# Performance work log

Hardware: AMD Instinct MI355X
Metric: run time of the kernel (lower is better)

The kernel has to match this reference:

```python
import jax, jax.numpy as jnp
import numpy as np

B, S, D, H, DK, DV, F, L, V = 2, 1024, 1024, 16, 64, 64, 4096, 4, 32000
PAD = 0
EPS = 1e-5


def posenc(seq_len, dim):
    # sinusoidal positional encoding (dim even)
    pos = jnp.arange(seq_len, dtype=jnp.float32)[:, None]
    div = jnp.exp(-(jnp.arange(0, dim, 2, dtype=jnp.float32) / dim) * np.log(10000.0))
    pe = jnp.zeros((seq_len, dim), jnp.float32)
    pe = pe.at[:, 0::2].set(jnp.sin(pos * div))
    pe = pe.at[:, 1::2].set(jnp.cos(pos * div))
    return pe


def layer_norm(x, g, b):
    mu = jnp.mean(x, axis=-1, keepdims=True)
    var = jnp.mean((x - mu) ** 2, axis=-1, keepdims=True)
    return (x - mu) / jnp.sqrt(var + EPS) * g + b


def setup_inputs() -> dict:
    key = jax.random.key(0)
    ks = jax.random.split(key, 10)
    n = lambda k, shape: jax.random.normal(k, shape, jnp.float32) * 0.02
    return {
        "tokens": jax.random.randint(ks[0], (B, S), 0, V),
        "emb": n(ks[1], (V, D)),
        "Wq": n(ks[2], (L, D, H * DK)), "bq": jnp.zeros((L, H * DK), jnp.float32),
        "Wk": n(ks[3], (L, D, H * DK)), "bk": jnp.zeros((L, H * DK), jnp.float32),
        "Wv": n(ks[4], (L, D, H * DV)), "bv": jnp.zeros((L, H * DV), jnp.float32),
        "Wo": n(ks[5], (L, H * DV, D)), "bo": jnp.zeros((L, D), jnp.float32),
        "ln1_g": jnp.ones((L, D), jnp.float32), "ln1_b": jnp.zeros((L, D), jnp.float32),
        "W1": n(ks[6], (L, D, F)),
        "W2": n(ks[7], (L, F, D)),
        "ln2_g": jnp.ones((L, D), jnp.float32), "ln2_b": jnp.zeros((L, D), jnp.float32),
    }


def reference(tokens, emb, Wq, bq, Wk, bk, Wv, bv, Wo, bo,
              ln1_g, ln1_b, W1, W2, ln2_g, ln2_b):
    x = emb[tokens] + posenc(S, D)                      # [B,S,D]
    # pad mask from key sequence: True where key token == PAD, broadcast over heads/queries
    mask = (tokens == PAD)[:, None, None, :]            # [B,1,1,S]
    scale = 1.0 / np.sqrt(DK)
    for l in range(L):
        residual = x
        q = (x @ Wq[l] + bq[l]).reshape(B, S, H, DK).transpose(0, 2, 1, 3)  # [B,H,S,DK]
        k = (x @ Wk[l] + bk[l]).reshape(B, S, H, DK).transpose(0, 2, 1, 3)
        v = (x @ Wv[l] + bv[l]).reshape(B, S, H, DV).transpose(0, 2, 1, 3)
        scores = jnp.einsum('bhqd,bhkd->bhqk', q, k) * scale                # [B,H,S,S]
        scores = jnp.where(mask, -1e9, scores)
        attn = jax.nn.softmax(scores, axis=-1)
        ctx = jnp.einsum('bhqk,bhkd->bhqd', attn, v)                        # [B,H,S,DV]
        ctx = ctx.transpose(0, 2, 1, 3).reshape(B, S, H * DV)
        x = layer_norm(residual + ctx @ Wo[l] + bo[l], ln1_g[l], ln1_b[l])
        # position-wise FFN (linear mode, no bias, exact GELU)
        h = jax.nn.gelu(x @ W1[l], approximate=False)
        x = layer_norm(x + h @ W2[l], ln2_g[l], ln2_b[l])
    return x
```

## Files before the change

### kernel.cpp

```cpp
#include <hip/hip_runtime.h>
#include <math.h>

#define S_  1024
#define D_  1024
#define Hh  16
#define DKk 64
#define Bb  2
#define Ff  4096
#define Ll  4

typedef __bf16 bf16_t;
using bf16x4 = __attribute__((ext_vector_type(4))) __bf16;
using bf16x8 = __attribute__((ext_vector_type(8))) __bf16;
using f32x4  = __attribute__((ext_vector_type(4))) float;

#define AS1 __attribute__((address_space(1)))
#define AS3 __attribute__((address_space(3)))

__device__ __forceinline__ void gld_lds16(const bf16_t* g, bf16_t* l)
{
    __builtin_amdgcn_global_load_lds((AS1 void*)g, (AS3 void*)l, 16, 0, 0);
}

__global__ __launch_bounds__(256) void embed_kernel(const int* __restrict__ tokens,
                                                    const float* __restrict__ emb,
                                                    float* __restrict__ X,
                                                    bf16_t* __restrict__ Xh)
{
    const int row = blockIdx.x;
    const int s   = row & (S_ - 1);
    const int tok = tokens[row];
    const float* e = emb + (size_t)tok * D_;
    const float LN10000 = 9.210340371976184f;
    #pragma unroll
    for (int i = 0; i < 4; ++i) {
        int d = threadIdx.x + 256 * i;
        int half = d >> 1;
        float div = expf(-((float)(2 * half) / (float)D_) * LN10000);
        float ang = (float)s * div;
        float pe = (d & 1) ? cosf(ang) : sinf(ang);
        float v = e[d] + pe;
        X [(size_t)row * D_ + d] = v;
        Xh[(size_t)row * D_ + d] = (bf16_t)v;
    }
}

__global__ __launch_bounds__(256) void transpose_cast_kernel(const float* __restrict__ in,
                                                             bf16_t* __restrict__ out,
                                                             int K, int N)
{
    __shared__ float T[32][33];
    const int n0 = blockIdx.x * 32;
    const int k0 = blockIdx.y * 32;
    const int t  = threadIdx.x;
    const int r  = t >> 3;
    const int c  = (t & 7) * 4;

    float4 v = *(const float4*)(in + (size_t)(k0 + r) * N + n0 + c);
    T[r][c + 0] = v.x; T[r][c + 1] = v.y; T[r][c + 2] = v.z; T[r][c + 3] = v.w;
    __syncthreads();

    bf16x4 o = { (bf16_t)T[c + 0][r], (bf16_t)T[c + 1][r],
                 (bf16_t)T[c + 2][r], (bf16_t)T[c + 3][r] };
    *(bf16x4*)(out + (size_t)(n0 + r) * K + k0 + c) = o;
}

__global__ __launch_bounds__(256) void concat_bias_kernel(const float* __restrict__ bq,
                                                          const float* __restrict__ bk,
                                                          const float* __restrict__ bv,
                                                          float* __restrict__ out)
{
    const int id = blockIdx.x * 256 + threadIdx.x;
    const int l  = id / 3072;
    const int j  = id % 3072;
    float v;
    if (j < 1024)      v = bq[l * 1024 + j];
    else if (j < 2048) v = bk[l * 1024 + j - 1024];
    else               v = bv[l * 1024 + j - 2048];
    out[id] = v;
}

template<int BN>
__global__ __launch_bounds__(256) void gemm_bf16_kernel(const bf16_t* __restrict__ A,
                                                        const bf16_t* __restrict__ Bt,
                                                        const float* __restrict__ bias,
                                                        void* __restrict__ Cv,
                                                        int N, int K, int flags)
{
    constexpr int NI = BN / 32;
    __shared__ bf16_t As[128 * 32];
    __shared__ bf16_t Bs[BN * 32];

    const int t    = threadIdx.x;
    const int w    = t >> 6;
    const int lane = t & 63;
    const int l15  = lane & 15;
    const int q8   = lane >> 4;
    const int wm   = w >> 1;
    const int wn   = w & 1;

    const int bm = blockIdx.y * 128;
    const int bn = blockIdx.x * BN;

    const int lr4 = lane >> 2;
    const int lc8 = (lane & 3) * 8;

    f32x4 acc[4][NI] = {};

    for (int k0 = 0; k0 < K; k0 += 32) {
        #pragma unroll
        for (int u = 0; u < 2; ++u) {
            const int row0 = w * 32 + u * 16;
            gld_lds16(A + (size_t)(bm + row0 + lr4) * K + k0 + lc8,
                      As + row0 * 32);
        }
        #pragma unroll
        for (int u = 0; u < BN / 64; ++u) {
            const int row0 = w * (BN / 4) + u * 16;
            gld_lds16(Bt + (size_t)(bn + row0 + lr4) * K + k0 + lc8,
                      Bs + row0 * 32);
        }
        __syncthreads();

        bf16x8 af[4], bf[NI];
        #pragma unroll
        for (int mi = 0; mi < 4; ++mi)
            af[mi] = *(const bf16x8*)(As + (wm * 64 + mi * 16 + l15) * 32 + q8 * 8);
        #pragma unroll
        for (int ni = 0; ni < NI; ++ni)
            bf[ni] = *(const bf16x8*)(Bs + (wn * (NI * 16) + ni * 16 + l15) * 32 + q8 * 8);

        #pragma unroll
        for (int mi = 0; mi < 4; ++mi)
            #pragma unroll
            for (int ni = 0; ni < NI; ++ni)
                acc[mi][ni] = __builtin_amdgcn_mfma_f32_16x16x32_bf16(
                                  af[mi], bf[ni], acc[mi][ni], 0, 0, 0);
        __syncthreads();
    }

    #pragma unroll
    for (int mi = 0; mi < 4; ++mi) {
        #pragma unroll
        for (int ni = 0; ni < NI; ++ni) {
            const int n = bn + wn * (NI * 16) + ni * 16 + l15;
            const float bv_ = (flags & 1) ? bias[n] : 0.f;
            #pragma unroll
            for (int r = 0; r < 4; ++r) {
                const int m = bm + wm * 64 + mi * 16 + q8 * 4 + r;
                float v = acc[mi][ni][r] + bv_;
                if (flags & 2) v = 0.5f * v * (1.0f + erff(v * 0.70710678118654752f));
                if (flags & 4) ((bf16_t*)Cv)[(size_t)m * N + n] = (bf16_t)v;
                else           ((float*) Cv)[(size_t)m * N + n] = v;
            }
        }
    }
}

#define AST 72
#define LDQ 3072

__global__ __launch_bounds__(256) void attn_mfma_kernel(const bf16_t* __restrict__ QKV,
                                                        const int* __restrict__ tokens,
                                                        bf16_t* __restrict__ Octx)
{
    const int qt = blockIdx.x;
    const int h  = blockIdx.y;
    const int b  = blockIdx.z;
    const int t    = threadIdx.x;
    const int wave = t >> 6;
    const int lane = t & 63;
    const int l15  = lane & 15;
    const int q8   = lane >> 4;

    __shared__ bf16_t Ks[64][AST];
    __shared__ bf16_t VsT[64][AST];
    __shared__ bf16_t Ps[4][16][AST];

    const bf16_t* Qp = QKV + 0;
    const bf16_t* Kp = QKV + 1024;
    const bf16_t* Vp = QKV + 2048;

    const int q0 = qt * 64 + wave * 16;
    bf16x8 qf0, qf1;
    {
        const bf16_t* qp = Qp + ((size_t)(b * S_ + q0 + l15)) * LDQ + h * 64 + q8 * 8;
        qf0 = *(const bf16x8*)(qp);
        qf1 = *(const bf16x8*)(qp + 32);
    }

    f32x4 Oacc[4] = {};
    float m_run[4], l_run[4];
    #pragma unroll
    for (int r = 0; r < 4; ++r) { m_run[r] = -INFINITY; l_run[r] = 0.f; }

    for (int jt = 0; jt < S_ / 64; ++jt) {
        __syncthreads();
        {
            const bf16_t* kb = Kp + ((size_t)(b * S_ + jt * 64)) * LDQ + h * 64;
            #pragma unroll
            for (int u = 0; u < 2; ++u) {
                int id = t + 256 * u;
                int r  = id >> 3;
                int c  = (id & 7) * 8;
                *(uint4*)&Ks[r][c] = *(const uint4*)(kb + (size_t)r * LDQ + c);
            }
        }
        {
            const bf16_t* vb = Vp + ((size_t)(b * S_ + jt * 64)) * LDQ + h * 64;
            const int j  = lane;
            const int d0 = wave * 16;
            #pragma unroll
            for (int u = 0; u < 2; ++u) {
                bf16x8 vv = *(const bf16x8*)(vb + (size_t)j * LDQ + d0 + u * 8);
                #pragma unroll
                for (int e = 0; e < 8; ++e)
                    VsT[d0 + u * 8 + e][j] = vv[e];
            }
        }
        __syncthreads();

        float sc[4][4];
        #pragma unroll
        for (int nt = 0; nt < 4; ++nt) {
            const bf16_t* kp = &Ks[nt * 16 + l15][q8 * 8];
            bf16x8 b0 = *(const bf16x8*)(kp);
            bf16x8 b1 = *(const bf16x8*)(kp + 32);
            f32x4 a = {};
            a = __builtin_amdgcn_mfma_f32_16x16x32_bf16(qf0, b0, a, 0, 0, 0);
            a = __builtin_amdgcn_mfma_f32_16x16x32_bf16(qf1, b1, a, 0, 0, 0);
            const int jg = jt * 64 + nt * 16 + l15;
            const float msk = (tokens[b * S_ + jg] == 0) ? -1e9f : 0.f;
            #pragma unroll
            for (int r = 0; r < 4; ++r) sc[nt][r] = a[r] * 0.125f + msk;
        }

        float alpha[4];
        #pragma unroll
        for (int r = 0; r < 4; ++r) {
            float mx = fmaxf(fmaxf(sc[0][r], sc[1][r]), fmaxf(sc[2][r], sc[3][r]));
            #pragma unroll
            for (int o = 1; o < 16; o <<= 1) mx = fmaxf(mx, __shfl_xor(mx, o));
            const float mn = fmaxf(m_run[r], mx);
            alpha[r] = __expf(m_run[r] - mn);
            m_run[r] = mn;
            float s = 0.f;
            #pragma unroll
            for (int nt = 0; nt < 4; ++nt) {
                float p = __expf(sc[nt][r] - mn);
                sc[nt][r] = p;
                s += p;
            }
            #pragma unroll
            for (int o = 1; o < 16; o <<= 1) s += __shfl_xor(s, o);
            l_run[r] = l_run[r] * alpha[r] + s;
        }

        #pragma unroll
        for (int nt = 0; nt < 4; ++nt)
            #pragma unroll
            for (int r = 0; r < 4; ++r)
                Ps[wave][q8 * 4 + r][nt * 16 + l15] = (bf16_t)sc[nt][r];

        bf16x8 pf0 = *(const bf16x8*)&Ps[wave][l15][q8 * 8];
        bf16x8 pf1 = *(const bf16x8*)&Ps[wave][l15][32 + q8 * 8];

        #pragma unroll
        for (int dt = 0; dt < 4; ++dt) {
            #pragma unroll
            for (int r = 0; r < 4; ++r) Oacc[dt][r] *= alpha[r];
            const bf16_t* vp = &VsT[dt * 16 + l15][q8 * 8];
            bf16x8 v0 = *(const bf16x8*)(vp);
            bf16x8 v1 = *(const bf16x8*)(vp + 32);
            Oacc[dt] = __builtin_amdgcn_mfma_f32_16x16x32_bf16(pf0, v0, Oacc[dt], 0, 0, 0);
            Oacc[dt] = __builtin_amdgcn_mfma_f32_16x16x32_bf16(pf1, v1, Oacc[dt], 0, 0, 0);
        }
    }

    #pragma unroll
    for (int dt = 0; dt < 4; ++dt) {
        #pragma unroll
        for (int r = 0; r < 4; ++r) {
            const int qg = q0 + q8 * 4 + r;
            Octx[((size_t)(b * S_ + qg)) * D_ + h * 64 + dt * 16 + l15] =
                (bf16_t)(Oacc[dt][r] / l_run[r]);
        }
    }
}

__global__ __launch_bounds__(256) void add_ln_kernel(const float* __restrict__ R,
                                                     const float* __restrict__ T,
                                                     const float* __restrict__ g,
                                                     const float* __restrict__ bta,
                                                     float* __restrict__ out,
                                                     bf16_t* __restrict__ outh)
{
    const int row = blockIdx.x;
    const int t = threadIdx.x;
    const float* r  = R + (size_t)row * D_;
    const float* tp = T + (size_t)row * D_;

    float v[4];
    float s = 0.f;
    #pragma unroll
    for (int i = 0; i < 4; ++i) {
        int d = t + 256 * i;
        v[i] = r[d] + tp[d];
        s += v[i];
    }

    __shared__ float red[8];
    #pragma unroll
    for (int o = 32; o > 0; o >>= 1) s += __shfl_xor(s, o);
    if ((t & 63) == 0) red[t >> 6] = s;
    __syncthreads();
    const float mean = (red[0] + red[1] + red[2] + red[3]) * (1.0f / D_);

    float vs = 0.f;
    #pragma unroll
    for (int i = 0; i < 4; ++i) { float d = v[i] - mean; vs += d * d; }
    #pragma unroll
    for (int o = 32; o > 0; o >>= 1) vs += __shfl_xor(vs, o);
    if ((t & 63) == 0) red[4 + (t >> 6)] = vs;
    __syncthreads();
    const float var = (red[4] + red[5] + red[6] + red[7]) * (1.0f / D_);
    const float inv = rsqrtf(var + 1e-5f);

    #pragma unroll
    for (int i = 0; i < 4; ++i) {
        int d = t + 256 * i;
        float o = (v[i] - mean) * inv * g[d] + bta[d];
        out [(size_t)row * D_ + d] = o;
        outh[(size_t)row * D_ + d] = (bf16_t)o;
    }
}

extern "C" void kernel_launch(void* const* d_in, const int* in_sizes, int n_in,
                              void* d_out, int out_size, void* d_ws, size_t ws_size,
                              hipStream_t stream)
{
    const int*   tokens = (const int*)  d_in[0];
    const float* emb    = (const float*)d_in[1];
    const float* Wq     = (const float*)d_in[2];
    const float* bq     = (const float*)d_in[3];
    const float* Wk     = (const float*)d_in[4];
    const float* bk     = (const float*)d_in[5];
    const float* Wv     = (const float*)d_in[6];
    const float* bv     = (const float*)d_in[7];
    const float* Wo     = (const float*)d_in[8];
    const float* bo     = (const float*)d_in[9];
    const float* ln1g   = (const float*)d_in[10];
    const float* ln1b   = (const float*)d_in[11];
    const float* W1     = (const float*)d_in[12];
    const float* W2     = (const float*)d_in[13];
    const float* ln2g   = (const float*)d_in[14];
    const float* ln2b   = (const float*)d_in[15];

    const int M = Bb * S_;
    const size_t MD = (size_t)M * D_;

    uint8_t* p = (uint8_t*)d_ws;
    float*  X     = (float*)p;           p += MD * 4;
    float*  T1    = (float*)p;           p += MD * 4;
    bf16_t* Xh    = (bf16_t*)p;          p += MD * 2;
    bf16_t* QKVh  = (bf16_t*)p;          p += (size_t)M * 3072 * 2;
    bf16_t* CTXh  = (bf16_t*)p;          p += MD * 2;
    bf16_t* HBh   = (bf16_t*)p;          p += (size_t)M * Ff * 2;
    bf16_t* WQKVt = (bf16_t*)p;          p += (size_t)3072 * D_ * 2;
    bf16_t* Wot   = (bf16_t*)p;          p += (size_t)D_ * D_ * 2;
    bf16_t* W1t   = (bf16_t*)p;          p += (size_t)Ff * D_ * 2;
    bf16_t* W2t   = (bf16_t*)p;          p += (size_t)D_ * Ff * 2;
    float*  bqkv  = (float*)p;           p += (size_t)Ll * 3072 * 4;

    embed_kernel<<<M, 256, 0, stream>>>(tokens, emb, X, Xh);
    concat_bias_kernel<<<Ll * 3072 / 256, 256, 0, stream>>>(bq, bk, bv, bqkv);

    for (int l = 0; l < Ll; ++l) {
        const float* Wq_l = Wq + (size_t)l * D_ * D_;
        const float* Wk_l = Wk + (size_t)l * D_ * D_;
        const float* Wv_l = Wv + (size_t)l * D_ * D_;
        const float* Wo_l = Wo + (size_t)l * D_ * D_;
        const float* W1_l = W1 + (size_t)l * D_ * Ff;
        const float* W2_l = W2 + (size_t)l * Ff * D_;

        dim3 tDD(D_ / 32, D_ / 32);
        transpose_cast_kernel<<<tDD, 256, 0, stream>>>(Wq_l, WQKVt,               D_, D_);
        transpose_cast_kernel<<<tDD, 256, 0, stream>>>(Wk_l, WQKVt + D_ * D_,     D_, D_);
        transpose_cast_kernel<<<tDD, 256, 0, stream>>>(Wv_l, WQKVt + 2 * D_ * D_, D_, D_);
        transpose_cast_kernel<<<tDD, 256, 0, stream>>>(Wo_l, Wot,                 D_, D_);
        transpose_cast_kernel<<<dim3(Ff / 32, D_ / 32), 256, 0, stream>>>(W1_l, W1t, D_, Ff);
        transpose_cast_kernel<<<dim3(D_ / 32, Ff / 32), 256, 0, stream>>>(W2_l, W2t, Ff, D_);

        gemm_bf16_kernel<128><<<dim3(3072 / 128, M / 128), 256, 0, stream>>>(
            Xh, WQKVt, bqkv + l * 3072, QKVh, 3072, D_, 1 | 4);

        attn_mfma_kernel<<<dim3(S_ / 64, Hh, Bb), 256, 0, stream>>>(QKVh, tokens, CTXh);

        gemm_bf16_kernel<64><<<dim3(D_ / 64, M / 128), 256, 0, stream>>>(
            CTXh, Wot, bo + (size_t)l * D_, T1, D_, D_, 1);

        add_ln_kernel<<<M, 256, 0, stream>>>(X, T1, ln1g + (size_t)l * D_,
                                             ln1b + (size_t)l * D_, X, Xh);

        gemm_bf16_kernel<128><<<dim3(Ff / 128, M / 128), 256, 0, stream>>>(
            Xh, W1t, nullptr, HBh, Ff, D_, 2 | 4);

        gemm_bf16_kernel<64><<<dim3(D_ / 64, M / 128), 256, 0, stream>>>(
            HBh, W2t, nullptr, T1, D_, Ff, 0);

        float* dst = (l == Ll - 1) ? (float*)d_out : X;
        add_ln_kernel<<<M, 256, 0, stream>>>(X, T1, ln2g + (size_t)l * D_,
                                             ln2b + (size_t)l * D_, dst, Xh);
    }
}
```

Measured before the change: 1.208 ms.

## Batch weight transposes up front and split-K the Wo and W2 GEMMs

Replaces the 24 per-layer weight transpose launches with three batched transpose kernels run once before the layer loop, storing all layers' bf16 transposed weights. Adds split-K to the Wo (2-way) and W2 (4-way) GEMMs, writing fp32 partials that add_ln sums, to put more blocks on the device for the narrow N=1024 outputs. The QKV GEMM switches to a 64-row tile for more blocks. This costs extra workspace and more partial-sum traffic through add_ln.

```diff
diff --git a/kernel.cpp b/kernel.cpp
--- a/kernel.cpp
+++ b/kernel.cpp
@@ -16,6 +16,8 @@
 
 #define AS1 __attribute__((address_space(1)))
 #define AS3 __attribute__((address_space(3)))
+
+#define MD_ ((size_t)2048 * 1024)
 
 __device__ __forceinline__ void gld_lds16(const bf16_t* g, bf16_t* l)
 {
@@ -45,16 +47,14 @@
     }
 }
 
-__global__ __launch_bounds__(256) void transpose_cast_kernel(const float* __restrict__ in,
-                                                             bf16_t* __restrict__ out,
-                                                             int K, int N)
+__device__ __forceinline__ void transpose_tile(const float* __restrict__ in,
+                                               bf16_t* __restrict__ out,
+                                               int K, int N, int n0, int k0)
 {
     __shared__ float T[32][33];
-    const int n0 = blockIdx.x * 32;
-    const int k0 = blockIdx.y * 32;
-    const int t  = threadIdx.x;
-    const int r  = t >> 3;
-    const int c  = (t & 7) * 4;
+    const int t = threadIdx.x;
+    const int r = t >> 3;
+    const int c = (t & 7) * 4;
 
     float4 v = *(const float4*)(in + (size_t)(k0 + r) * N + n0 + c);
     T[r][c + 0] = v.x; T[r][c + 1] = v.y; T[r][c + 2] = v.z; T[r][c + 3] = v.w;
@@ -63,6 +63,31 @@
     bf16x4 o = { (bf16_t)T[c + 0][r], (bf16_t)T[c + 1][r],
                  (bf16_t)T[c + 2][r], (bf16_t)T[c + 3][r] };
     *(bf16x4*)(out + (size_t)(n0 + r) * K + k0 + c) = o;
+}
+
+__global__ __launch_bounds__(256) void transpose_qkvo_kernel(const float* __restrict__ Wq,
+                                                             const float* __restrict__ Wk,
+                                                             const float* __restrict__ Wv,
+                                                             const float* __restrict__ Wo,
+                                                             bf16_t* __restrict__ WQKVt,
+                                                             bf16_t* __restrict__ Wot)
+{
+    const int z = blockIdx.z;
+    const int l = z >> 2;
+    const int which = z & 3;
+    const float* src = (which == 0 ? Wq : which == 1 ? Wk : which == 2 ? Wv : Wo)
+                       + (size_t)l * D_ * D_;
+    bf16_t* dst = (which < 3) ? WQKVt + (size_t)l * 3072 * D_ + (size_t)which * D_ * D_
+                              : Wot + (size_t)l * D_ * D_;
+    transpose_tile(src, dst, D_, D_, blockIdx.x * 32, blockIdx.y * 32);
+}
+
+__global__ __launch_bounds__(256) void transpose_batch_kernel(const float* __restrict__ in,
+                                                              bf16_t* __restrict__ out,
+                                                              int K, int N)
+{
+    const size_t off = (size_t)blockIdx.z * K * N;
+    transpose_tile(in + off, out + off, K, N, blockIdx.x * 32, blockIdx.y * 32);
 }
 
 __global__ __launch_bounds__(256) void concat_bias_kernel(const float* __restrict__ bq,
@@ -80,15 +105,16 @@
     out[id] = v;
 }
 
-template<int BN>
+template<int BM, int BN>
 __global__ __launch_bounds__(256) void gemm_bf16_kernel(const bf16_t* __restrict__ A,
                                                         const bf16_t* __restrict__ Bt,
                                                         const float* __restrict__ bias,
                                                         void* __restrict__ Cv,
-                                                        int N, int K, int flags)
-{
+                                                        int N, int Kfull, int Kc, int flags)
+{
+    constexpr int MI = BM / 32;
     constexpr int NI = BN / 32;
-    __shared__ bf16_t As[128 * 32];
+    __shared__ bf16_t As[BM * 32];
     __shared__ bf16_t Bs[BN * 32];
 
     const int t    = threadIdx.x;
@@ -99,39 +125,42 @@
     const int wm   = w >> 1;
     const int wn   = w & 1;
 
-    const int bm = blockIdx.y * 128;
+    const int bm = blockIdx.y * BM;
     const int bn = blockIdx.x * BN;
+    const int kz = blockIdx.z;
 
     const int lr4 = lane >> 2;
     const int lc8 = (lane & 3) * 8;
 
-    f32x4 acc[4][NI] = {};
-
-    for (int k0 = 0; k0 < K; k0 += 32) {
-        #pragma unroll
-        for (int u = 0; u < 2; ++u) {
-            const int row0 = w * 32 + u * 16;
-            gld_lds16(A + (size_t)(bm + row0 + lr4) * K + k0 + lc8,
+    f32x4 acc[MI][NI] = {};
+
+    const int kbeg = kz * Kc;
+    const int kend = kbeg + Kc;
+    for (int k0 = kbeg; k0 < kend; k0 += 32) {
+        #pragma unroll
+        for (int u = 0; u < BM / 64; ++u) {
+            const int row0 = w * (BM / 4) + u * 16;
+            gld_lds16(A + (size_t)(bm + row0 + lr4) * Kfull + k0 + lc8,
                       As + row0 * 32);
         }
         #pragma unroll
         for (int u = 0; u < BN / 64; ++u) {
             const int row0 = w * (BN / 4) + u * 16;
-            gld_lds16(Bt + (size_t)(bn + row0 + lr4) * K + k0 + lc8,
+            gld_lds16(Bt + (size_t)(bn + row0 + lr4) * Kfull + k0 + lc8,
                       Bs + row0 * 32);
         }
         __syncthreads();
 
-        bf16x8 af[4], bf[NI];
-        #pragma unroll
-        for (int mi = 0; mi < 4; ++mi)
-            af[mi] = *(const bf16x8*)(As + (wm * 64 + mi * 16 + l15) * 32 + q8 * 8);
+        bf16x8 af[MI], bf[NI];
+        #pragma unroll
+        for (int mi = 0; mi < MI; ++mi)
+            af[mi] = *(const bf16x8*)(As + (wm * (BM / 2) + mi * 16 + l15) * 32 + q8 * 8);
         #pragma unroll
         for (int ni = 0; ni < NI; ++ni)
-            bf[ni] = *(const bf16x8*)(Bs + (wn * (NI * 16) + ni * 16 + l15) * 32 + q8 * 8);
-
-        #pragma unroll
-        for (int mi = 0; mi < 4; ++mi)
+            bf[ni] = *(const bf16x8*)(Bs + (wn * (BN / 2) + ni * 16 + l15) * 32 + q8 * 8);
+
+        #pragma unroll
+        for (int mi = 0; mi < MI; ++mi)
             #pragma unroll
             for (int ni = 0; ni < NI; ++ni)
                 acc[mi][ni] = __builtin_amdgcn_mfma_f32_16x16x32_bf16(
@@ -139,19 +168,20 @@
         __syncthreads();
     }
 
-    #pragma unroll
-    for (int mi = 0; mi < 4; ++mi) {
+    float* Cf = (float*)Cv + (size_t)kz * 2048 * N;
+    #pragma unroll
+    for (int mi = 0; mi < MI; ++mi) {
         #pragma unroll
         for (int ni = 0; ni < NI; ++ni) {
-            const int n = bn + wn * (NI * 16) + ni * 16 + l15;
-            const float bv_ = (flags & 1) ? bias[n] : 0.f;
+            const int n = bn + wn * (BN / 2) + ni * 16 + l15;
+            const float bv_ = ((flags & 1) && kz == 0) ? bias[n] : 0.f;
             #pragma unroll
             for (int r = 0; r < 4; ++r) {
-                const int m = bm + wm * 64 + mi * 16 + q8 * 4 + r;
+                const int m = bm + wm * (BM / 2) + mi * 16 + q8 * 4 + r;
                 float v = acc[mi][ni][r] + bv_;
                 if (flags & 2) v = 0.5f * v * (1.0f + erff(v * 0.70710678118654752f));
                 if (flags & 4) ((bf16_t*)Cv)[(size_t)m * N + n] = (bf16_t)v;
-                else           ((float*) Cv)[(size_t)m * N + n] = v;
+                else           Cf[(size_t)m * N + n] = v;
             }
         }
     }
@@ -288,6 +318,7 @@
     }
 }
 
+template<int NP>
 __global__ __launch_bounds__(256) void add_ln_kernel(const float* __restrict__ R,
                                                      const float* __restrict__ T,
                                                      const float* __restrict__ g,
@@ -305,8 +336,11 @@
     #pragma unroll
     for (int i = 0; i < 4; ++i) {
         int d = t + 256 * i;
-        v[i] = r[d] + tp[d];
-        s += v[i];
+        float acc = r[d];
+        #pragma unroll
+        for (int p = 0; p < NP; ++p) acc += tp[p * MD_ + d];
+        v[i] = acc;
+        s += acc;
     }
 
     __shared__ float red[8];
@@ -361,55 +395,48 @@
 
     uint8_t* p = (uint8_t*)d_ws;
     float*  X     = (float*)p;           p += MD * 4;
-    float*  T1    = (float*)p;           p += MD * 4;
+    float*  T1    = (float*)p;           p += MD * 4 * 4;
     bf16_t* Xh    = (bf16_t*)p;          p += MD * 2;
     bf16_t* QKVh  = (bf16_t*)p;          p += (size_t)M * 3072 * 2;
     bf16_t* CTXh  = (bf16_t*)p;          p += MD * 2;
     bf16_t* HBh   = (bf16_t*)p;          p += (size_t)M * Ff * 2;
-    bf16_t* WQKVt = (bf16_t*)p;          p += (size_t)3072 * D_ * 2;
-    bf16_t* Wot   = (bf16_t*)p;          p += (size_t)D_ * D_ * 2;
-    bf16_t* W1t   = (bf16_t*)p;          p += (size_t)Ff * D_ * 2;
-    bf16_t* W2t   = (bf16_t*)p;          p += (size_t)D_ * Ff * 2;
+    bf16_t* WQKVt = (bf16_t*)p;          p += (size_t)Ll * 3072 * D_ * 2;
+    bf16_t* Wot   = (bf16_t*)p;          p += (size_t)Ll * D_ * D_ * 2;
+    bf16_t* W1t   = (bf16_t*)p;          p += (size_t)Ll * Ff * D_ * 2;
+    bf16_t* W2t   = (bf16_t*)p;          p += (size_t)Ll * D_ * Ff * 2;
     float*  bqkv  = (float*)p;           p += (size_t)Ll * 3072 * 4;
 
     embed_kernel<<<M, 256, 0, stream>>>(tokens, emb, X, Xh);
     concat_bias_kernel<<<Ll * 3072 / 256, 256, 0, stream>>>(bq, bk, bv, bqkv);
+    transpose_qkvo_kernel<<<dim3(32, 32, 16), 256, 0, stream>>>(Wq, Wk, Wv, Wo, WQKVt, Wot);
+    transpose_batch_kernel<<<dim3(Ff / 32, D_ / 32, Ll), 256, 0, stream>>>(W1, W1t, D_, Ff);
+    transpose_batch_kernel<<<dim3(D_ / 32, Ff / 32, Ll), 256, 0, stream>>>(W2, W2t, Ff, D_);
 
     for (int l = 0; l < Ll; ++l) {
-        const float* Wq_l = Wq + (size_t)l * D_ * D_;
-        const float* Wk_l = Wk + (size_t)l * D_ * D_;
-        const float* Wv_l = Wv + (size_t)l * D_ * D_;
-        const float* Wo_l = Wo + (size_t)l * D_ * D_;
-        const float* W1_l = W1 + (size_t)l * D_ * Ff;
-        const float* W2_l = W2 + (size_t)l * Ff * D_;
-
-        dim3 tDD(D_ / 32, D_ / 32);
-        transpose_cast_kernel<<<tDD, 256, 0, stream>>>(Wq_l, WQKVt,               D_, D_);
-        transpose_cast_kernel<<<tDD, 256, 0, stream>>>(Wk_l, WQKVt + D_ * D_,     D_, D_);
-        transpose_cast_kernel<<<tDD, 256, 0, stream>>>(Wv_l, WQKVt + 2 * D_ * D_, D_, D_);
-        transpose_cast_kernel<<<tDD, 256, 0, stream>>>(Wo_l, Wot,                 D_, D_);
-        transpose_cast_kernel<<<dim3(Ff / 32, D_ / 32), 256, 0, stream>>>(W1_l, W1t, D_, Ff);
-        transpose_cast_kernel<<<dim3(D_ / 32, Ff / 32), 256, 0, stream>>>(W2_l, W2t, Ff, D_);
-
-        gemm_bf16_kernel<128><<<dim3(3072 / 128, M / 128), 256, 0, stream>>>(
-            Xh, WQKVt, bqkv + l * 3072, QKVh, 3072, D_, 1 | 4);
+        const bf16_t* WQKVt_l = WQKVt + (size_t)l * 3072 * D_;
+        const bf16_t* Wot_l   = Wot   + (size_t)l * D_ * D_;
+        const bf16_t* W1t_l   = W1t   + (size_t)l * Ff * D_;
+        const bf16_t* W2t_l   = W2t   + (size_t)l * D_ * Ff;
+
+        gemm_bf16_kernel<64, 128><<<dim3(3072 / 128, M / 64), 256, 0, stream>>>(
+            Xh, WQKVt_l, bqkv + l * 3072, QKVh, 3072, D_, D_, 1 | 4);
 
         attn_mfma_kernel<<<dim3(S_ / 64, Hh, Bb), 256, 0, stream>>>(QKVh, tokens, CTXh);
 
-        gemm_bf16_kernel<64><<<dim3(D_ / 64, M / 128), 256, 0, stream>>>(
-            CTXh, Wot, bo + (size_t)l * D_, T1, D_, D_, 1);
-
-        add_ln_kernel<<<M, 256, 0, stream>>>(X, T1, ln1g + (size_t)l * D_,
-                                             ln1b + (size_t)l * D_, X, Xh);
-
-        gemm_bf16_kernel<128><<<dim3(Ff / 128, M / 128), 256, 0, stream>>>(
-            Xh, W1t, nullptr, HBh, Ff, D_, 2 | 4);
-
-        gemm_bf16_kernel<64><<<dim3(D_ / 64, M / 128), 256, 0, stream>>>(
-            HBh, W2t, nullptr, T1, D_, Ff, 0);
+        gemm_bf16_kernel<128, 64><<<dim3(D_ / 64, M / 128, 2), 256, 0, stream>>>(
+            CTXh, Wot_l, bo + (size_t)l * D_, T1, D_, D_, D_ / 2, 1);
+
+        add_ln_kernel<2><<<M, 256, 0, stream>>>(X, T1, ln1g + (size_t)l * D_,
+                                                ln1b + (size_t)l * D_, X, Xh);
+
+        gemm_bf16_kernel<128, 128><<<dim3(Ff / 128, M / 128), 256, 0, stream>>>(
+            Xh, W1t_l, nullptr, HBh, Ff, D_, D_, 2 | 4);
+
+        gemm_bf16_kernel<128, 64><<<dim3(D_ / 64, M / 128, 4), 256, 0, stream>>>(
+            HBh, W2t_l, nullptr, T1, D_, Ff, Ff / 4, 0);
 
         float* dst = (l == Ll - 1) ? (float*)d_out : X;
-        add_ln_kernel<<<M, 256, 0, stream>>>(X, T1, ln2g + (size_t)l * D_,
-                                             ln2b + (size_t)l * D_, dst, Xh);
-    }
-}
+        add_ln_kernel<4><<<M, 256, 0, stream>>>(X, T1, ln2g + (size_t)l * D_,
+                                                ln2b + (size_t)l * D_, dst, Xh);
+    }
+}
```

New measurement: 1.068 ms. 11.6% less time.
